# Kernel optimization log

Hardware: AMD Instinct MI355X
Metric: run time of the kernel (lower is better)

The kernel has to match this reference:

```python
import jax, jax.numpy as jnp
import numpy as np

DEPTH, DIM, HEADS, DH = 6, 1024, 16, 64
INNER = int(DIM * 2 * 4 / 3)        # 2730 (GEGLU FFN inner dim)
INNER2 = INNER * 2                  # 5460
B, N = 2, 1024
NUM_BUCKETS, MAX_DIST = 32, 128
ALPHA = 0.1                         # grad_shrink alpha (identity in fwd)


def setup_inputs() -> dict:
    key = jax.random.key(0)
    ks = jax.random.split(key, 12)
    s = 0.02
    return {
        "x": jax.random.normal(ks[0], (B, N, DIM), jnp.float32),
        "rel_emb": jax.random.normal(ks[1], (NUM_BUCKETS, HEADS), jnp.float32) * s,
        "qn_g": jnp.ones((DEPTH, DIM), jnp.float32),
        "wq": jax.random.normal(ks[2], (DEPTH, DIM, HEADS * DH), jnp.float32) * s,
        "wkv": jax.random.normal(ks[3], (DEPTH, DIM, 2 * DH), jnp.float32) * s,
        "wo": jax.random.normal(ks[4], (DEPTH, HEADS * DH, DIM), jnp.float32) * s,
        "ln1_g": jnp.ones((DEPTH, DIM), jnp.float32),
        "w1": jax.random.normal(ks[5], (DEPTH, DIM, INNER2), jnp.float32) * s,
        "convw": jax.random.normal(ks[6], (DEPTH, INNER2, 3), jnp.float32) * s,
        "ln2_g": jnp.ones((DEPTH, INNER), jnp.float32),
        "w2": jax.random.normal(ks[7], (DEPTH, INNER, DIM), jnp.float32) * s,
        "final_g": jnp.ones((DIM,), jnp.float32),
    }


def _ln(x, g):
    m = jnp.mean(x, axis=-1, keepdims=True)
    v = jnp.mean(jnp.square(x - m), axis=-1, keepdims=True)
    return (x - m) * jax.lax.rsqrt(v + 1e-5) * g


def _rel_pos_bias(rel_emb, n):
    # T5-style buckets, causal variant (as in RelativePositionBias.forward)
    q_pos = jnp.arange(n)
    k_pos = jnp.arange(n)
    npos = jnp.maximum(q_pos[:, None] - k_pos[None, :], 0)   # -relative_position, clamped
    max_exact = NUM_BUCKETS // 2
    nf = jnp.maximum(npos, 1).astype(jnp.float32)
    val_large = max_exact + (jnp.log(nf / max_exact) / np.log(MAX_DIST / max_exact)
                             * (NUM_BUCKETS - max_exact)).astype(jnp.int32)
    val_large = jnp.minimum(val_large, NUM_BUCKETS - 1)
    bucket = jnp.where(npos < max_exact, npos, val_large)
    return rel_emb[bucket].transpose(2, 0, 1)  # [h, i, j]


def _forward(x, rel_emb, qn_g, wq, wkv, wo, ln1_g, w1, convw, ln2_g, w2, final_g):
    b, n, _ = x.shape
    x = x * ALPHA + jax.lax.stop_gradient(x) * (1.0 - ALPHA)  # grad_shrink
    bias = _rel_pos_bias(rel_emb, n)                          # [h, n, n]
    causal = jnp.triu(jnp.ones((n, n), bool), 1)
    neg = -jnp.finfo(x.dtype).max
    scale = DH ** -0.5

    for l in range(DEPTH):
        # --- causal self-attention (single-head K/V) ---
        h = _ln(x, qn_g[l])
        q = (h @ wq[l]).reshape(b, n, HEADS, DH).transpose(0, 2, 1, 3) * scale  # [b,h,n,d]
        kv = h @ wkv[l]
        k, v = kv[..., :DH], kv[..., DH:]                                       # [b,n,d]
        sim = jnp.einsum('bhid,bjd->bhij', q, k) + bias
        sim = jnp.where(causal, neg, sim)
        attn = jax.nn.softmax(sim, axis=-1)
        o = jnp.einsum('bhij,bjd->bhid', attn, v)
        o = o.transpose(0, 2, 1, 3).reshape(b, n, HEADS * DH)
        x = o @ wo[l] + x

        # --- FFN: LN -> Linear -> causal depthwise conv -> GEGLU -> LN -> Linear ---
        h = _ln(x, ln1_g[l]) @ w1[l]                 # [b, n, INNER2]
        hp = jnp.pad(h, ((0, 0), (2, 0), (0, 0)))    # causal pad
        w = convw[l]                                  # [INNER2, 3]
        h = hp[:, :-2] * w[:, 0] + hp[:, 1:-1] * w[:, 1] + hp[:, 2:] * w[:, 2]
        a, gate = h[..., :INNER], h[..., INNER:]
        h = jax.nn.gelu(gate, approximate=False) * a
        h = _ln(h, ln2_g[l]) @ w2[l]
        x = h + x

    return _ln(x, final_g)


def reference(x, rel_emb, qn_g, wq, wkv, wo, ln1_g, w1, convw, ln2_g, w2, final_g):
    return _forward(x, rel_emb, qn_g, wq, wkv, wo, ln1_g, w1, convw, ln2_g, w2, final_g)
```

## Files before the change

### kernel.cpp

```cpp
#include <hip/hip_runtime.h>
#include <math.h>

#define DEPTH 6
#define DIM 1024
#define HEADS 16
#define DH 64
#define INNER 2730
#define INNER2 5460
#define INNERP 2752
#define N1P 5504
#define BATCH 2
#define SEQ 1024
#define TOK (BATCH*SEQ)
#define QKVW 1152

#define OFF_WO 1179648ull
#define OFF_W1 2228224ull
#define OFF_W2 7864320ull
#define LWT    10682368ull
#define TILES_PER_LAYER 2608

typedef unsigned short ushort;
typedef __attribute__((ext_vector_type(8))) short short8;
typedef __attribute__((ext_vector_type(4))) short short4v;
typedef __attribute__((ext_vector_type(4))) unsigned short ushort4v;
typedef __attribute__((ext_vector_type(2))) unsigned short ushort2v;
typedef __attribute__((ext_vector_type(4))) float floatx4;

__device__ inline ushort f2bf(float f) {
  unsigned int u = __float_as_uint(f);
  u += 0x7FFF + ((u >> 16) & 1);
  return (ushort)(u >> 16);
}
__device__ inline float bf2f(ushort u) {
  return __uint_as_float(((unsigned int)u) << 16);
}

__device__ inline void gload_lds16(const ushort* g, ushort* l) {
  __builtin_amdgcn_global_load_lds(
      (const __attribute__((address_space(1))) unsigned int*)g,
      (__attribute__((address_space(3))) unsigned int*)l, 16, 0, 0);
}

__global__ void bias_frag_kernel(const float* __restrict__ rel_emb, float* __restrict__ bias_c) {
  int h = blockIdx.x >> 4, dq = blockIdx.x & 15;
  for (int i = threadIdx.x; i < 4096; i += 256) {
    int reg = i & 3, col = (i >> 2) & 15, j = (i >> 6) & 3, rowgrp = i >> 8;
    int row = rowgrp * 4 + reg, colg = j * 16 + col;
    int d = dq * 64 + row - colg;
    d = d < 0 ? 0 : (d > 1023 ? 1023 : d);
    int bucket;
    if (d < 16) {
      bucket = d;
    } else {
      float nf = (float)d;
      int vl = 16 + (int)(logf(nf / 16.0f) / 2.0794415416798357f * 16.0f);
      bucket = vl < 31 ? vl : 31;
    }
    bias_c[((size_t)(h * 16 + dq)) * 4096 + i] = rel_emb[bucket * HEADS + h];
  }
}

__device__ inline void transpose_body(const float* __restrict__ W, ushort* __restrict__ Wt,
                                      int K, int N, int Kp, int Np, float scale,
                                      int k0, int n0, size_t dst_row0) {
  __shared__ float t[64][65];
  int tid = threadIdx.x;
  int kl = tid >> 4, nc = (tid & 15) * 4;
#pragma unroll
  for (int it = 0; it < 4; it++) {
    int k = kl + it * 16;
    int gk = k0 + k, gn = n0 + nc;
    floatx4 v = {0.f, 0.f, 0.f, 0.f};
    if (gk < K && gn < N) v = *(const floatx4*)&W[(size_t)gk * N + gn];
    t[nc + 0][k] = v[0] * scale;
    t[nc + 1][k] = v[1] * scale;
    t[nc + 2][k] = v[2] * scale;
    t[nc + 3][k] = v[3] * scale;
  }
  __syncthreads();
  int nr = tid >> 3, q = tid & 7;
#pragma unroll
  for (int it = 0; it < 2; it++) {
    int n = nr + it * 32;
    if (n0 + n < Np) {
      short8 p;
#pragma unroll
      for (int e = 0; e < 8; e++) p[e] = (short)f2bf(t[n][q * 8 + e]);
      *(short8*)&Wt[(dst_row0 + n) * Kp + k0 + q * 8] = p;
    }
  }
}

__global__ __launch_bounds__(256) void transpose_vec(const float* __restrict__ W,
                                                     ushort* __restrict__ Wt,
                                                     int K, int N, int Kp, int Np, float scale) {
  transpose_body(W, Wt, K, N, Kp, Np, scale, blockIdx.y * 64, blockIdx.x * 64,
                 (size_t)blockIdx.x * 64);
}

__global__ __launch_bounds__(256) void transpose_qkv(const float* __restrict__ wq,
                                                     const float* __restrict__ wkv,
                                                     ushort* __restrict__ Wt) {
  int bx = blockIdx.x;
  if (bx < 16) {
    transpose_body(wq, Wt, 1024, 1024, 1024, 1024, 0.125f, blockIdx.y * 64, bx * 64,
                   (size_t)bx * 64);
  } else {
    transpose_body(wkv, Wt, 1024, 128, 1024, 128, 1.0f, blockIdx.y * 64, (bx - 16) * 64,
                   (size_t)1024 + (bx - 16) * 64);
  }
}

__global__ __launch_bounds__(256) void transpose_all(const float* __restrict__ wq,
                                                     const float* __restrict__ wkv,
                                                     const float* __restrict__ wo,
                                                     const float* __restrict__ w1,
                                                     const float* __restrict__ w2,
                                                     ushort* __restrict__ wtall) {
  int t = blockIdx.x;
  int l = t / TILES_PER_LAYER, r = t % TILES_PER_LAYER;
  ushort* base = wtall + (size_t)l * LWT;
  if (r < 288) {
    int bx = r % 18, by = r / 18;
    if (bx < 16)
      transpose_body(wq + (size_t)l * 1024 * 1024, base, 1024, 1024, 1024, 1024,
                     0.125f, by * 64, bx * 64, (size_t)bx * 64);
    else
      transpose_body(wkv + (size_t)l * 1024 * 128, base, 1024, 128, 1024, 128,
                     1.0f, by * 64, (bx - 16) * 64, 1024 + (size_t)(bx - 16) * 64);
  } else if (r < 544) {
    int q = r - 288, bx = q & 15, by = q >> 4;
    transpose_body(wo + (size_t)l * 1024 * 1024, base + OFF_WO, 1024, 1024, 1024, 1024,
                   1.0f, by * 64, bx * 64, (size_t)bx * 64);
  } else if (r < 1920) {
    int q = r - 544, bx = q % 86, by = q / 86;
    transpose_body(w1 + (size_t)l * 1024 * 5460, base + OFF_W1, 1024, 5460, 1024, 5504,
                   1.0f, by * 64, bx * 64, (size_t)bx * 64);
  } else {
    int q = r - 1920, bx = q & 15, by = q >> 4;
    transpose_body(w2 + (size_t)l * 2730 * 1024, base + OFF_W2, 2730, 1024, 2752, 1024,
                   1.0f, by * 64, bx * 64, (size_t)bx * 64);
  }
}

template <typename OutT>
__global__ __launch_bounds__(256) void ln1024(const float* __restrict__ in,
                                              const float* __restrict__ g,
                                              OutT* __restrict__ out) {
  int row = blockIdx.x;
  int tid = threadIdx.x;
  floatx4 v = *(const floatx4*)&in[(size_t)row * 1024 + tid * 4];
  float s = v[0] + v[1] + v[2] + v[3];
  float ss = v[0] * v[0] + v[1] * v[1] + v[2] * v[2] + v[3] * v[3];
#pragma unroll
  for (int off = 32; off; off >>= 1) {
    s  += __shfl_down(s, off, 64);
    ss += __shfl_down(ss, off, 64);
  }
  __shared__ float l1[4], l2[4];
  int wid = tid >> 6, lane = tid & 63;
  if (lane == 0) { l1[wid] = s; l2[wid] = ss; }
  __syncthreads();
  if (tid == 0) {
    float a = l1[0] + l1[1] + l1[2] + l1[3];
    float bb = l2[0] + l2[1] + l2[2] + l2[3];
    float m = a * (1.0f / 1024.0f);
    float var = bb * (1.0f / 1024.0f) - m * m;
    l1[0] = m;
    l2[0] = rsqrtf(var + 1e-5f);
  }
  __syncthreads();
  float m = l1[0], r = l2[0];
  floatx4 gv = *(const floatx4*)&g[tid * 4];
  if constexpr (sizeof(OutT) == 2) {
    short4v p;
#pragma unroll
    for (int e = 0; e < 4; e++) p[e] = (short)f2bf((v[e] - m) * r * gv[e]);
    *(short4v*)&out[(size_t)row * 1024 + tid * 4] = p;
  } else {
    floatx4 p;
#pragma unroll
    for (int e = 0; e < 4; e++) p[e] = (v[e] - m) * r * gv[e];
    *(floatx4*)&out[(size_t)row * 1024 + tid * 4] = p;
  }
}

template <bool ADD, typename OutT>
__global__ __launch_bounds__(256) void gemm_mfma128(const ushort* __restrict__ A,
                                                    const ushort* __restrict__ Bt,
                                                    const float* __restrict__ Cin,
                                                    OutT* __restrict__ C,
                                                    int N, int K, float scale) {
  __shared__ ushort Als[128 * 64];
  __shared__ ushort Bls[128 * 64];
  int tid = threadIdx.x;
  int w = tid >> 6, lane = tid & 63;
  int wr = w >> 1, wc = w & 1;
  size_t row0 = (size_t)blockIdx.y * 128, col0 = (size_t)blockIdx.x * 128;

  const ushort* Ag = A + (row0 + w * 32 + (lane >> 3)) * (size_t)K + (lane & 7) * 8;
  const ushort* Bg = Bt + (col0 + w * 32 + (lane >> 3)) * (size_t)K + (lane & 7) * 8;
  ushort* Al = Als + w * 32 * 64;
  ushort* Bl = Bls + w * 32 * 64;

  floatx4 acc[4][4];
#pragma unroll
  for (int i = 0; i < 4; i++)
#pragma unroll
    for (int j = 0; j < 4; j++) { floatx4 z = {0.f, 0.f, 0.f, 0.f}; acc[i][j] = z; }

  int mrow = lane & 15, kq = (lane >> 4) * 8;
  for (int k0 = 0; k0 < K; k0 += 64) {
#pragma unroll
    for (int r = 0; r < 4; r++) {
      gload_lds16(Ag + (size_t)(r * 8) * K + k0, Al + r * 8 * 64);
      gload_lds16(Bg + (size_t)(r * 8) * K + k0, Bl + r * 8 * 64);
    }
    __syncthreads();
#pragma unroll
    for (int kk = 0; kk < 64; kk += 32) {
      short8 a[4], b[4];
#pragma unroll
      for (int i = 0; i < 4; i++)
        a[i] = *(const short8*)&Als[(wr * 64 + i * 16 + mrow) * 64 + kk + kq];
#pragma unroll
      for (int j = 0; j < 4; j++)
        b[j] = *(const short8*)&Bls[(wc * 64 + j * 16 + mrow) * 64 + kk + kq];
#pragma unroll
      for (int i = 0; i < 4; i++)
#pragma unroll
        for (int j = 0; j < 4; j++)
          acc[i][j] = __builtin_amdgcn_mfma_f32_16x16x32_bf16(a[i], b[j], acc[i][j], 0, 0, 0);
    }
    __syncthreads();
  }
  int orow = (lane >> 4) * 4, ocol = lane & 15;
#pragma unroll
  for (int i = 0; i < 4; i++) {
#pragma unroll
    for (int ii = 0; ii < 4; ii++) {
      size_t gr = row0 + wr * 64 + i * 16 + orow + ii;
#pragma unroll
      for (int j = 0; j < 4; j++) {
        size_t gc = col0 + wc * 64 + j * 16 + ocol;
        float v = acc[i][j][ii] * scale;
        if (ADD) v += Cin[gr * N + gc];
        if constexpr (sizeof(OutT) == 2) C[gr * N + gc] = f2bf(v);
        else C[gr * N + gc] = v;
      }
    }
  }
}

template <bool ADD, typename OutT>
__global__ __launch_bounds__(256) void gemm_mfma64(const ushort* __restrict__ A,
                                                   const ushort* __restrict__ Bt,
                                                   const float* __restrict__ Cin,
                                                   OutT* __restrict__ C,
                                                   int N, int K, float scale) {
  __shared__ ushort Als[128 * 64];
  __shared__ ushort Bls[64 * 64];
  int tid = threadIdx.x;
  int w = tid >> 6, lane = tid & 63;
  size_t row0 = (size_t)blockIdx.y * 128, col0 = (size_t)blockIdx.x * 64;

  const ushort* Ag = A + (row0 + w * 32 + (lane >> 3)) * (size_t)K + (lane & 7) * 8;
  const ushort* Bg = Bt + (col0 + w * 16 + (lane >> 3)) * (size_t)K + (lane & 7) * 8;
  ushort* Al = Als + w * 32 * 64;
  ushort* Bl = Bls + w * 16 * 64;

  floatx4 acc[2][4];
#pragma unroll
  for (int i = 0; i < 2; i++)
#pragma unroll
    for (int j = 0; j < 4; j++) { floatx4 z = {0.f, 0.f, 0.f, 0.f}; acc[i][j] = z; }

  int mrow = lane & 15, kq = (lane >> 4) * 8;
  for (int k0 = 0; k0 < K; k0 += 64) {
#pragma unroll
    for (int r = 0; r < 4; r++)
      gload_lds16(Ag + (size_t)(r * 8) * K + k0, Al + r * 8 * 64);
#pragma unroll
    for (int r = 0; r < 2; r++)
      gload_lds16(Bg + (size_t)(r * 8) * K + k0, Bl + r * 8 * 64);
    __syncthreads();
#pragma unroll
    for (int kk = 0; kk < 64; kk += 32) {
      short8 a[2], b[4];
#pragma unroll
      for (int i = 0; i < 2; i++)
        a[i] = *(const short8*)&Als[(w * 32 + i * 16 + mrow) * 64 + kk + kq];
#pragma unroll
      for (int j = 0; j < 4; j++)
        b[j] = *(const short8*)&Bls[(j * 16 + mrow) * 64 + kk + kq];
#pragma unroll
      for (int i = 0; i < 2; i++)
#pragma unroll
        for (int j = 0; j < 4; j++)
          acc[i][j] = __builtin_amdgcn_mfma_f32_16x16x32_bf16(a[i], b[j], acc[i][j], 0, 0, 0);
    }
    __syncthreads();
  }
  int orow = (lane >> 4) * 4, ocol = lane & 15;
#pragma unroll
  for (int i = 0; i < 2; i++) {
#pragma unroll
    for (int ii = 0; ii < 4; ii++) {
      size_t gr = row0 + w * 32 + i * 16 + orow + ii;
#pragma unroll
      for (int j = 0; j < 4; j++) {
        size_t gc = col0 + j * 16 + ocol;
        float v = acc[i][j][ii] * scale;
        if (ADD) v += Cin[gr * N + gc];
        if constexpr (sizeof(OutT) == 2) C[gr * N + gc] = f2bf(v);
        else C[gr * N + gc] = v;
      }
    }
  }
}

__global__ __launch_bounds__(256) void convglu_ln(const ushort* __restrict__ h1,
                                                  const float* __restrict__ cw,
                                                  const float* __restrict__ lng,
                                                  ushort* __restrict__ out) {
  int t = blockIdx.x;
  int n = t & (SEQ - 1);
  int tid = threadIdx.x;
  const ushort* r0 = h1 + (size_t)t * N1P;
  float vals[3][4];
  float s = 0.f, ss = 0.f;
#pragma unroll
  for (int it = 0; it < 3; it++) {
    int c = (it * 256 + tid) * 4;
#pragma unroll
    for (int e = 0; e < 4; e++) vals[it][e] = 0.f;
    if (c < INNER) {
      ushort4v a2 = *(const ushort4v*)&r0[c];
      ushort4v a1 = {0, 0, 0, 0}, a0 = {0, 0, 0, 0};
      if (n >= 1) a1 = *(const ushort4v*)&r0[c - N1P];
      if (n >= 2) a0 = *(const ushort4v*)&r0[c - 2 * N1P];
      int cg = c + INNER;
      ushort2v g2a = *(const ushort2v*)&r0[cg];
      ushort2v g2b = *(const ushort2v*)&r0[cg + 2];
      ushort2v g1a = {0, 0}, g1b = {0, 0}, g0a = {0, 0}, g0b = {0, 0};
      if (n >= 1) { g1a = *(const ushort2v*)&r0[cg - N1P]; g1b = *(const ushort2v*)&r0[cg + 2 - N1P]; }
      if (n >= 2) { g0a = *(const ushort2v*)&r0[cg - 2 * N1P]; g0b = *(const ushort2v*)&r0[cg + 2 - 2 * N1P]; }
      const floatx4* cwa = (const floatx4*)(cw + (size_t)c * 3);
      floatx4 f0 = cwa[0], f1 = cwa[1], f2 = cwa[2];
      float wa[12] = {f0[0], f0[1], f0[2], f0[3], f1[0], f1[1], f1[2], f1[3],
                      f2[0], f2[1], f2[2], f2[3]};
#pragma unroll
      for (int e = 0; e < 4; e++) {
        int ce = c + e;
        if (ce < INNER) {
          float av = bf2f(a0[e]) * wa[e * 3] + bf2f(a1[e]) * wa[e * 3 + 1] +
                     bf2f(a2[e]) * wa[e * 3 + 2];
          int cge = ce + INNER;
          float w0g = cw[cge * 3], w1g = cw[cge * 3 + 1], w2g = cw[cge * 3 + 2];
          float g0f = bf2f(e < 2 ? g0a[e & 1] : g0b[e & 1]);
          float g1f = bf2f(e < 2 ? g1a[e & 1] : g1b[e & 1]);
          float g2f = bf2f(e < 2 ? g2a[e & 1] : g2b[e & 1]);
          float gvv = g0f * w0g + g1f * w1g + g2f * w2g;
          float gl = 0.5f * gvv * (1.0f + erff(gvv * 0.70710678118654752f));
          float val = gl * av;
          vals[it][e] = val;
          s += val;
          ss += val * val;
        }
      }
    }
  }
#pragma unroll
  for (int off = 32; off; off >>= 1) {
    s  += __shfl_down(s, off, 64);
    ss += __shfl_down(ss, off, 64);
  }
  __shared__ float l1[4], l2[4];
  int wid = tid >> 6, lane = tid & 63;
  if (lane == 0) { l1[wid] = s; l2[wid] = ss; }
  __syncthreads();
  if (tid == 0) {
    float a = l1[0] + l1[1] + l1[2] + l1[3];
    float bb = l2[0] + l2[1] + l2[2] + l2[3];
    float m = a * (1.0f / INNER);
    float var = bb * (1.0f / INNER) - m * m;
    l1[0] = m;
    l2[0] = rsqrtf(var + 1e-5f);
  }
  __syncthreads();
  float m = l1[0], r = l2[0];
#pragma unroll
  for (int it = 0; it < 3; it++) {
    int c = (it * 256 + tid) * 4;
    if (c < INNERP) {
      short4v p;
#pragma unroll
      for (int e = 0; e < 4; e++) {
        int ce = c + e;
        p[e] = (ce < INNER) ? (short)f2bf((vals[it][e] - m) * r * lng[ce]) : (short)0;
      }
      *(short4v*)&out[(size_t)t * INNERP + c] = p;
    }
  }
}

__global__ __launch_bounds__(256) void attn_mfma(const ushort* __restrict__ qkv,
                                                 const float* __restrict__ bias_c,
                                                 ushort* __restrict__ o) {
  __shared__ ushort Ks[64 * 72];
  __shared__ ushort Vt[64 * 72];
  __shared__ ushort Ps[64 * 72];
  __shared__ float arow[64];
  int tid = threadIdx.x;
  int lane = tid & 63, w = tid >> 6;
  int quad = lane >> 4, col = lane & 15;
  int b = blockIdx.x >> 4, h = blockIdx.x & 15;
  int y = blockIdx.y;
  int qt = (y < 8) ? (15 - y) : (y - 8);

  const ushort* qrow = qkv + (size_t)(b * SEQ + qt * 64 + w * 16 + col) * QKVW + h * 64;
  short8 qa[2];
  qa[0] = *(const short8*)&qrow[quad * 8];
  qa[1] = *(const short8*)&qrow[32 + quad * 8];

  float m_[4], l_[4];
  floatx4 oacc[4];
#pragma unroll
  for (int r = 0; r < 4; r++) { m_[r] = -1e30f; l_[r] = 0.f; }
#pragma unroll
  for (int mt = 0; mt < 4; mt++) { floatx4 z = {0.f, 0.f, 0.f, 0.f}; oacc[mt] = z; }

  for (int kc = 0; kc <= qt; kc++) {
    const ushort* kvb = qkv + (size_t)(b * SEQ + kc * 64) * QKVW;
#pragma unroll
    for (int it = 0; it < 2; it++) {
      int r = lane;
      int c8 = w + it * 4;
      short8 kk8 = *(const short8*)&kvb[(size_t)r * QKVW + 1024 + c8 * 8];
      *(short8*)&Ks[r * 72 + c8 * 8] = kk8;
      short8 vv = *(const short8*)&kvb[(size_t)r * QKVW + 1088 + c8 * 8];
#pragma unroll
      for (int e = 0; e < 8; e++) Vt[(c8 * 8 + e) * 72 + r] = (ushort)vv[e];
    }
    __syncthreads();

    floatx4 sarr[4];
#pragma unroll
    for (int j = 0; j < 4; j++) { floatx4 z = {0.f, 0.f, 0.f, 0.f}; sarr[j] = z; }
#pragma unroll
    for (int kk = 0; kk < 2; kk++) {
#pragma unroll
      for (int j = 0; j < 4; j++) {
        short8 kb = *(const short8*)&Ks[(j * 16 + col) * 72 + kk * 32 + quad * 8];
        sarr[j] = __builtin_amdgcn_mfma_f32_16x16x32_bf16(qa[kk], kb, sarr[j], 0, 0, 0);
      }
    }

    int dq = qt - kc;
    const floatx4* bc = (const floatx4*)(bias_c + ((size_t)(h * 16 + dq) * 4096 + (w * 4 + quad) * 256));
    float pv[4][4];
#pragma unroll
    for (int j = 0; j < 4; j++) {
      floatx4 bf = bc[j * 16 + col];
#pragma unroll
      for (int reg = 0; reg < 4; reg++) {
        float v = sarr[j][reg] + bf[reg];
        if (dq == 0 && (j * 16 + col) > (w * 16 + quad * 4 + reg)) v = -1e30f;
        pv[j][reg] = v;
      }
    }

#pragma unroll
    for (int reg = 0; reg < 4; reg++) {
      float cm = fmaxf(fmaxf(pv[0][reg], pv[1][reg]), fmaxf(pv[2][reg], pv[3][reg]));
      cm = fmaxf(cm, __shfl_xor(cm, 1, 64));
      cm = fmaxf(cm, __shfl_xor(cm, 2, 64));
      cm = fmaxf(cm, __shfl_xor(cm, 4, 64));
      cm = fmaxf(cm, __shfl_xor(cm, 8, 64));
      float nm = fmaxf(m_[reg], cm);
      float alpha = __expf(m_[reg] - nm);
      float rs = 0.f;
#pragma unroll
      for (int j = 0; j < 4; j++) {
        float e = __expf(pv[j][reg] - nm);
        pv[j][reg] = e;
        rs += e;
      }
      rs += __shfl_xor(rs, 1, 64);
      rs += __shfl_xor(rs, 2, 64);
      rs += __shfl_xor(rs, 4, 64);
      rs += __shfl_xor(rs, 8, 64);
      l_[reg] = l_[reg] * alpha + rs;
      m_[reg] = nm;
      if (col == 0) arow[w * 16 + quad * 4 + reg] = alpha;
    }

#pragma unroll
    for (int j = 0; j < 4; j++)
#pragma unroll
      for (int reg = 0; reg < 4; reg++)
        Ps[(w * 16 + quad * 4 + reg) * 72 + j * 16 + col] = f2bf(pv[j][reg]);

    asm volatile("s_waitcnt lgkmcnt(0)" ::: "memory");
    float aval = arow[w * 16 + col];
#pragma unroll
    for (int mt = 0; mt < 4; mt++) oacc[mt] *= aval;

#pragma unroll
    for (int kk = 0; kk < 2; kk++) {
      short8 pb = *(const short8*)&Ps[(w * 16 + col) * 72 + kk * 32 + quad * 8];
#pragma unroll
      for (int mt = 0; mt < 4; mt++) {
        short8 va = *(const short8*)&Vt[(mt * 16 + col) * 72 + kk * 32 + quad * 8];
        oacc[mt] = __builtin_amdgcn_mfma_f32_16x16x32_bf16(va, pb, oacc[mt], 0, 0, 0);
      }
    }
    __syncthreads();
  }

#pragma unroll
  for (int reg = 0; reg < 4; reg++)
    if (col == 0) arow[w * 16 + quad * 4 + reg] = 1.0f / l_[reg];
  asm volatile("s_waitcnt lgkmcnt(0)" ::: "memory");
  float lv = arow[w * 16 + col];
  size_t obase = (size_t)(b * SEQ + qt * 64 + w * 16 + col) * 1024 + h * 64;
#pragma unroll
  for (int mt = 0; mt < 4; mt++) {
    short4v pk;
#pragma unroll
    for (int reg = 0; reg < 4; reg++) pk[reg] = (short)f2bf(oacc[mt][reg] * lv);
    *(short4v*)&o[obase + mt * 16 + quad * 4] = pk;
  }
}

extern "C" void kernel_launch(void* const* d_in, const int* in_sizes, int n_in,
                              void* d_out, int out_size, void* d_ws, size_t ws_size,
                              hipStream_t stream) {
  const float* x_in    = (const float*)d_in[0];
  const float* rel_emb = (const float*)d_in[1];
  const float* qn_g    = (const float*)d_in[2];
  const float* wq      = (const float*)d_in[3];
  const float* wkv     = (const float*)d_in[4];
  const float* wo      = (const float*)d_in[5];
  const float* ln1_g   = (const float*)d_in[6];
  const float* w1      = (const float*)d_in[7];
  const float* convw   = (const float*)d_in[8];
  const float* ln2_g   = (const float*)d_in[9];
  const float* w2      = (const float*)d_in[10];
  const float* final_g = (const float*)d_in[11];
  float* out = (float*)d_out;

  float* xbuf   = (float*)d_ws;
  float* bias_c = xbuf + (size_t)TOK * DIM;
  ushort* hbuf  = (ushort*)(bias_c + (size_t)16 * 16 * 4096);
  ushort* obuf  = hbuf + (size_t)TOK * DIM;
  ushort* qkvbuf = obuf + (size_t)TOK * DIM;
  ushort* h1buf = qkvbuf + (size_t)TOK * QKVW;
  ushort* gbuf  = h1buf + (size_t)TOK * N1P;
  ushort* wtall = gbuf + (size_t)TOK * INNERP;

  size_t need = (size_t)((char*)(wtall + 6ull * LWT) - (char*)d_ws);
  bool big = ws_size >= need;

  bias_frag_kernel<<<256, 256, 0, stream>>>(rel_emb, bias_c);
  if (big)
    transpose_all<<<6 * TILES_PER_LAYER, 256, 0, stream>>>(wq, wkv, wo, w1, w2, wtall);

  for (int l = 0; l < DEPTH; l++) {
    const float* xres = (l == 0) ? x_in : xbuf;
    const ushort *wtq, *wto, *wt1, *wt2;
    if (big) {
      const ushort* bl = wtall + (size_t)l * LWT;
      wtq = bl; wto = bl + OFF_WO; wt1 = bl + OFF_W1; wt2 = bl + OFF_W2;
    } else {
      wtq = wto = wt1 = wt2 = wtall;
    }

    ln1024<ushort><<<TOK, 256, 0, stream>>>(xres, qn_g + l * DIM, hbuf);
    if (!big)
      transpose_qkv<<<dim3(18, 16), 256, 0, stream>>>(
          wq + (size_t)l * DIM * DIM, wkv + (size_t)l * DIM * 128, (ushort*)wtall);
    gemm_mfma64<false, ushort><<<dim3(18, 16), 256, 0, stream>>>(
        hbuf, wtq, nullptr, qkvbuf, QKVW, DIM, 1.0f);
    attn_mfma<<<dim3(BATCH * HEADS, 16), 256, 0, stream>>>(qkvbuf, bias_c, obuf);
    if (!big)
      transpose_vec<<<dim3(16, 16), 256, 0, stream>>>(
          wo + (size_t)l * DIM * DIM, (ushort*)wtall, DIM, DIM, DIM, DIM, 1.0f);
    gemm_mfma64<true, float><<<dim3(16, 16), 256, 0, stream>>>(
        obuf, wto, xres, xbuf, DIM, DIM, 1.0f);
    ln1024<ushort><<<TOK, 256, 0, stream>>>(xbuf, ln1_g + l * DIM, hbuf);
    if (!big)
      transpose_vec<<<dim3(86, 16), 256, 0, stream>>>(
          w1 + (size_t)l * DIM * INNER2, (ushort*)wtall, DIM, INNER2, DIM, N1P, 1.0f);
    gemm_mfma128<false, ushort><<<dim3(43, 16), 256, 0, stream>>>(
        hbuf, wt1, nullptr, h1buf, N1P, DIM, 1.0f);
    convglu_ln<<<TOK, 256, 0, stream>>>(
        h1buf, convw + (size_t)l * INNER2 * 3, ln2_g + l * INNER, gbuf);
    if (!big)
      transpose_vec<<<dim3(16, 43), 256, 0, stream>>>(
          w2 + (size_t)l * INNER * DIM, (ushort*)wtall, INNER, DIM, INNERP, DIM, 1.0f);
    gemm_mfma64<true, float><<<dim3(16, 16), 256, 0, stream>>>(
        gbuf, wt2, xbuf, xbuf, DIM, INNERP, 1.0f);
  }
  ln1024<float><<<TOK, 256, 0, stream>>>(xbuf, final_g, out);
}
```

Measured before the change: 1.673 ms.

## Use 64x64 GEMM tiles for narrow GEMMs and 128-row weight transpose tiles

The narrow-N GEMMs (QKV, Wo, W2) now use 64x64 output tiles, with each wave owning one 16-column slice, in place of 128x64 tiles. This doubles the number of blocks so more CUs are busy on the 2048-token problem. The weight transpose kernel now processes 128 K-rows per tile, which halves the block count in the one-time conversion. The trade-off is less operand reuse per block and fewer MFMAs per LDS load, so arithmetic intensity drops.

New measurement: 1.635 ms. -2.3%, faster.

```diff
diff --git a/kernel.cpp b/kernel.cpp
--- a/kernel.cpp
+++ b/kernel.cpp
@@ -18,7 +18,7 @@
 #define OFF_W1 2228224ull
 #define OFF_W2 7864320ull
 #define LWT    10682368ull
-#define TILES_PER_LAYER 2608
+#define TILES_PER_LAYER 1312
 
 typedef unsigned short ushort;
 typedef __attribute__((ext_vector_type(8))) short short8;
@@ -112,6 +112,44 @@
   }
 }
 
+__device__ inline void transpose_body128(const float* __restrict__ W, ushort* __restrict__ Wt,
+                                         int K, int N, int Kp, int Np, float scale,
+                                         int k0, int n0, size_t dst_row0) {
+  __shared__ float t[64][129];
+  int tid = threadIdx.x;
+  int kl = tid >> 4, nc = (tid & 15) * 4;
+#pragma unroll
+  for (int it = 0; it < 8; it++) {
+    int k = kl + it * 16;
+    int gk = k0 + k, gn = n0 + nc;
+    floatx4 v = {0.f, 0.f, 0.f, 0.f};
+    if (gk < K && gn < N) v = *(const floatx4*)&W[(size_t)gk * N + gn];
+    t[nc + 0][k] = v[0] * scale;
+    t[nc + 1][k] = v[1] * scale;
+    t[nc + 2][k] = v[2] * scale;
+    t[nc + 3][k] = v[3] * scale;
+  }
+  __syncthreads();
+  int nr = tid >> 3, q = tid & 7;
+#pragma unroll
+  for (int p = 0; p < 2; p++) {
+    int n = nr + p * 32;
+    if (n0 + n < Np) {
+      size_t rbase = (dst_row0 + n) * (size_t)Kp + k0;
+#pragma unroll
+      for (int it8 = 0; it8 < 2; it8++) {
+        int k = it8 * 64 + q * 8;
+        if (k0 + k < Kp) {
+          short8 pk;
+#pragma unroll
+          for (int e = 0; e < 8; e++) pk[e] = (short)f2bf(t[n][k + e]);
+          *(short8*)&Wt[rbase + k] = pk;
+        }
+      }
+    }
+  }
+}
+
 __global__ __launch_bounds__(256) void transpose_all(const float* __restrict__ wq,
                                                      const float* __restrict__ wkv,
                                                      const float* __restrict__ wo,
@@ -121,26 +159,28 @@
   int t = blockIdx.x;
   int l = t / TILES_PER_LAYER, r = t % TILES_PER_LAYER;
   ushort* base = wtall + (size_t)l * LWT;
-  if (r < 288) {
-    int bx = r % 18, by = r / 18;
-    if (bx < 16)
-      transpose_body(wq + (size_t)l * 1024 * 1024, base, 1024, 1024, 1024, 1024,
-                     0.125f, by * 64, bx * 64, (size_t)bx * 64);
-    else
-      transpose_body(wkv + (size_t)l * 1024 * 128, base, 1024, 128, 1024, 128,
-                     1.0f, by * 64, (bx - 16) * 64, 1024 + (size_t)(bx - 16) * 64);
-  } else if (r < 544) {
-    int q = r - 288, bx = q & 15, by = q >> 4;
-    transpose_body(wo + (size_t)l * 1024 * 1024, base + OFF_WO, 1024, 1024, 1024, 1024,
-                   1.0f, by * 64, bx * 64, (size_t)bx * 64);
-  } else if (r < 1920) {
-    int q = r - 544, bx = q % 86, by = q / 86;
-    transpose_body(w1 + (size_t)l * 1024 * 5460, base + OFF_W1, 1024, 5460, 1024, 5504,
-                   1.0f, by * 64, bx * 64, (size_t)bx * 64);
+  if (r < 144) {
+    if (r < 128) {
+      int bx = r & 15, by = r >> 4;
+      transpose_body128(wq + (size_t)l * 1024 * 1024, base, 1024, 1024, 1024, 1024,
+                        0.125f, by * 128, bx * 64, (size_t)bx * 64);
+    } else {
+      int q = r - 128, bx = q & 1, by = q >> 1;
+      transpose_body128(wkv + (size_t)l * 1024 * 128, base, 1024, 128, 1024, 128,
+                        1.0f, by * 128, bx * 64, 1024 + (size_t)bx * 64);
+    }
+  } else if (r < 272) {
+    int q = r - 144, bx = q & 15, by = q >> 4;
+    transpose_body128(wo + (size_t)l * 1024 * 1024, base + OFF_WO, 1024, 1024, 1024, 1024,
+                      1.0f, by * 128, bx * 64, (size_t)bx * 64);
+  } else if (r < 960) {
+    int q = r - 272, bx = q % 86, by = q / 86;
+    transpose_body128(w1 + (size_t)l * 1024 * 5460, base + OFF_W1, 1024, 5460, 1024, 5504,
+                      1.0f, by * 128, bx * 64, (size_t)bx * 64);
   } else {
-    int q = r - 1920, bx = q & 15, by = q >> 4;
-    transpose_body(w2 + (size_t)l * 2730 * 1024, base + OFF_W2, 2730, 1024, 2752, 1024,
-                   1.0f, by * 64, bx * 64, (size_t)bx * 64);
+    int q = r - 960, bx = q & 15, by = q >> 4;
+    transpose_body128(w2 + (size_t)l * 2730 * 1024, base + OFF_W2, 2730, 1024, 2752, 1024,
+                      1.0f, by * 128, bx * 64, (size_t)bx * 64);
   }
 }
 
@@ -254,68 +294,56 @@
 }
 
 template <bool ADD, typename OutT>
-__global__ __launch_bounds__(256) void gemm_mfma64(const ushort* __restrict__ A,
-                                                   const ushort* __restrict__ Bt,
-                                                   const float* __restrict__ Cin,
-                                                   OutT* __restrict__ C,
-                                                   int N, int K, float scale) {
-  __shared__ ushort Als[128 * 64];
+__global__ __launch_bounds__(256) void gemm64x64(const ushort* __restrict__ A,
+                                                 const ushort* __restrict__ Bt,
+                                                 const float* __restrict__ Cin,
+                                                 OutT* __restrict__ C,
+                                                 int N, int K, float scale) {
+  __shared__ ushort Als[64 * 64];
   __shared__ ushort Bls[64 * 64];
   int tid = threadIdx.x;
   int w = tid >> 6, lane = tid & 63;
-  size_t row0 = (size_t)blockIdx.y * 128, col0 = (size_t)blockIdx.x * 64;
-
-  const ushort* Ag = A + (row0 + w * 32 + (lane >> 3)) * (size_t)K + (lane & 7) * 8;
-  const ushort* Bg = Bt + (col0 + w * 16 + (lane >> 3)) * (size_t)K + (lane & 7) * 8;
-  ushort* Al = Als + w * 32 * 64;
-  ushort* Bl = Bls + w * 16 * 64;
-
-  floatx4 acc[2][4];
-#pragma unroll
-  for (int i = 0; i < 2; i++)
-#pragma unroll
-    for (int j = 0; j < 4; j++) { floatx4 z = {0.f, 0.f, 0.f, 0.f}; acc[i][j] = z; }
+  size_t row0 = (size_t)blockIdx.y * 64, col0 = (size_t)blockIdx.x * 64;
+
+  const ushort* Ag = A + (row0 + (tid >> 3)) * (size_t)K + (tid & 7) * 8;
+  const ushort* Bg = Bt + (col0 + (tid >> 3)) * (size_t)K + (tid & 7) * 8;
+  ushort* Al = Als + (tid >> 3) * 64 + (tid & 7) * 8;
+  ushort* Bl = Bls + (tid >> 3) * 64 + (tid & 7) * 8;
+
+  floatx4 acc[4];
+#pragma unroll
+  for (int i = 0; i < 4; i++) { floatx4 z = {0.f, 0.f, 0.f, 0.f}; acc[i] = z; }
 
   int mrow = lane & 15, kq = (lane >> 4) * 8;
   for (int k0 = 0; k0 < K; k0 += 64) {
 #pragma unroll
-    for (int r = 0; r < 4; r++)
-      gload_lds16(Ag + (size_t)(r * 8) * K + k0, Al + r * 8 * 64);
-#pragma unroll
-    for (int r = 0; r < 2; r++)
-      gload_lds16(Bg + (size_t)(r * 8) * K + k0, Bl + r * 8 * 64);
+    for (int p = 0; p < 2; p++) {
+      gload_lds16(Ag + (size_t)(p * 32) * K + k0, Al + p * 32 * 64);
+      gload_lds16(Bg + (size_t)(p * 32) * K + k0, Bl + p * 32 * 64);
+    }
     __syncthreads();
 #pragma unroll
     for (int kk = 0; kk < 64; kk += 32) {
-      short8 a[2], b[4];
-#pragma unroll
-      for (int i = 0; i < 2; i++)
-        a[i] = *(const short8*)&Als[(w * 32 + i * 16 + mrow) * 64 + kk + kq];
-#pragma unroll
-      for (int j = 0; j < 4; j++)
-        b[j] = *(const short8*)&Bls[(j * 16 + mrow) * 64 + kk + kq];
-#pragma unroll
-      for (int i = 0; i < 2; i++)
-#pragma unroll
-        for (int j = 0; j < 4; j++)
-          acc[i][j] = __builtin_amdgcn_mfma_f32_16x16x32_bf16(a[i], b[j], acc[i][j], 0, 0, 0);
+      short8 b = *(const short8*)&Bls[(w * 16 + mrow) * 64 + kk + kq];
+#pragma unroll
+      for (int i = 0; i < 4; i++) {
+        short8 a = *(const short8*)&Als[(i * 16 + mrow) * 64 + kk + kq];
+        acc[i] = __builtin_amdgcn_mfma_f32_16x16x32_bf16(a, b, acc[i], 0, 0, 0);
+      }
     }
     __syncthreads();
   }
   int orow = (lane >> 4) * 4, ocol = lane & 15;
 #pragma unroll
-  for (int i = 0; i < 2; i++) {
+  for (int i = 0; i < 4; i++) {
 #pragma unroll
     for (int ii = 0; ii < 4; ii++) {
-      size_t gr = row0 + w * 32 + i * 16 + orow + ii;
-#pragma unroll
-      for (int j = 0; j < 4; j++) {
-        size_t gc = col0 + j * 16 + ocol;
-        float v = acc[i][j][ii] * scale;
-        if (ADD) v += Cin[gr * N + gc];
-        if constexpr (sizeof(OutT) == 2) C[gr * N + gc] = f2bf(v);
-        else C[gr * N + gc] = v;
-      }
+      size_t gr = row0 + i * 16 + orow + ii;
+      size_t gc = col0 + w * 16 + ocol;
+      float v = acc[i][ii] * scale;
+      if (ADD) v += Cin[gr * N + gc];
+      if constexpr (sizeof(OutT) == 2) C[gr * N + gc] = f2bf(v);
+      else C[gr * N + gc] = v;
     }
   }
 }
@@ -581,13 +609,13 @@
     if (!big)
       transpose_qkv<<<dim3(18, 16), 256, 0, stream>>>(
           wq + (size_t)l * DIM * DIM, wkv + (size_t)l * DIM * 128, (ushort*)wtall);
-    gemm_mfma64<false, ushort><<<dim3(18, 16), 256, 0, stream>>>(
+    gemm64x64<false, ushort><<<dim3(18, 32), 256, 0, stream>>>(
         hbuf, wtq, nullptr, qkvbuf, QKVW, DIM, 1.0f);
     attn_mfma<<<dim3(BATCH * HEADS, 16), 256, 0, stream>>>(qkvbuf, bias_c, obuf);
     if (!big)
       transpose_vec<<<dim3(16, 16), 256, 0, stream>>>(
           wo + (size_t)l * DIM * DIM, (ushort*)wtall, DIM, DIM, DIM, DIM, 1.0f);
-    gemm_mfma64<true, float><<<dim3(16, 16), 256, 0, stream>>>(
+    gemm64x64<true, float><<<dim3(16, 32), 256, 0, stream>>>(
         obuf, wto, xres, xbuf, DIM, DIM, 1.0f);
     ln1024<ushort><<<TOK, 256, 0, stream>>>(xbuf, ln1_g + l * DIM, hbuf);
     if (!big)
@@ -600,7 +628,7 @@
     if (!big)
       transpose_vec<<<dim3(16, 43), 256, 0, stream>>>(
           w2 + (size_t)l * INNER * DIM, (ushort*)wtall, INNER, DIM, INNERP, DIM, 1.0f);
-    gemm_mfma64<true, float><<<dim3(16, 16), 256, 0, stream>>>(
+    gemm64x64<true, float><<<dim3(16, 32), 256, 0, stream>>>(
         gbuf, wt2, xbuf, xbuf, DIM, INNERP, 1.0f);
   }
   ln1024<float><<<TOK, 256, 0, stream>>>(xbuf, final_g, out);
```
